# Performance work log

Hardware: AMD Instinct MI355X
Metric: run time of the kernel (lower is better)

Reference implementation:

```python
import jax, jax.numpy as jnp
import numpy as np
from jax import lax

HIDDEN = 512

def _rnn_layer(xs, W_ih, W_hh, b):
    # xs: [B,T,F] -> ys: [B,T,H]; h_t = tanh(x_t W_ih^T + b + h_{t-1} W_hh^T)
    B = xs.shape[0]
    xp = jnp.einsum('btf,hf->bth', xs, W_ih) + b  # precompute input projections
    def step(h, xp_t):
        h = jnp.tanh(xp_t + h @ W_hh.T)
        return h, h
    h0 = jnp.zeros((B, W_hh.shape[0]), dtype=xs.dtype)
    _, ys = lax.scan(step, h0, xp.transpose(1, 0, 2))  # scan over time
    return ys.transpose(1, 0, 2)


def setup_inputs() -> dict:
    key = jax.random.key(0)
    ks = jax.random.split(key, 16)
    B, T, F, H, M, C = 128, 1024, 24, HIDDEN, 1024, 8
    s = 0.05  # small init to keep tanh unsaturated
    inp = {
        'x': jax.random.normal(ks[0], (B, T, F), jnp.float32),
        'W_ih0': jax.random.normal(ks[1], (H, F), jnp.float32) * s,
        'W_hh0': jax.random.normal(ks[2], (H, H), jnp.float32) * s,
        'b_ih0': jnp.zeros((H,), jnp.float32),
        'b_hh0': jnp.zeros((H,), jnp.float32),
        'W_ih1': jax.random.normal(ks[3], (H, H), jnp.float32) * s,
        'W_hh1': jax.random.normal(ks[4], (H, H), jnp.float32) * s,
        'b_ih1': jnp.zeros((H,), jnp.float32),
        'b_hh1': jnp.zeros((H,), jnp.float32),
        'W_ih2': jax.random.normal(ks[5], (H, H), jnp.float32) * s,
        'W_hh2': jax.random.normal(ks[6], (H, H), jnp.float32) * s,
        'b_ih2': jnp.zeros((H,), jnp.float32),
        'b_hh2': jnp.zeros((H,), jnp.float32),
        'W1': jax.random.normal(ks[7], (M, H), jnp.float32) * s,
        'b1': jnp.zeros((M,), jnp.float32),
        'W2': jax.random.normal(ks[8], (C, M), jnp.float32) * s,
        'b2': jnp.zeros((C,), jnp.float32),
    }
    return inp


def reference(x, W_ih0, W_hh0, b_ih0, b_hh0, W_ih1, W_hh1, b_ih1, b_hh1,
              W_ih2, W_hh2, b_ih2, b_hh2, W1, b1, W2, b2):
    h = _rnn_layer(x, W_ih0, W_hh0, b_ih0 + b_hh0)
    h = _rnn_layer(h, W_ih1, W_hh1, b_ih1 + b_hh1)
    h = _rnn_layer(h, W_ih2, W_hh2, b_ih2 + b_hh2)
    last = h[:, -1, :]  # [B,H] last timestep of top layer
    z = last @ W1.T + b1
    z = jax.nn.silu(z)
    return z @ W2.T + b2
```

## Files before the change

kernel.cpp:

```cpp
#include <hip/hip_runtime.h>
#include <cstdint>
#include <cstddef>


typedef _Float16 half_t;
typedef __attribute__((ext_vector_type(2))) _Float16 half2_t;
typedef __attribute__((ext_vector_type(8))) _Float16 frag8;
typedef __attribute__((ext_vector_type(4))) float    frag4;

union U32H2 { unsigned u; half2_t h2; };

__device__ __forceinline__ float dot2(unsigned a, unsigned b, float c) {
#if __has_builtin(__builtin_amdgcn_fdot2)
    U32H2 ua; ua.u = a; U32H2 ub; ub.u = b;
    return __builtin_amdgcn_fdot2(ua.h2, ub.h2, c, false);
#else
    U32H2 ua; ua.u = a; U32H2 ub; ub.u = b;
    c += (float)ua.h2.x * (float)ub.h2.x;
    c += (float)ua.h2.y * (float)ub.h2.y;
    return c;
#endif
}

__device__ __forceinline__ float fast_tanh(float x) {
    float ax = __builtin_fabsf(x);
    float e  = __expf(-2.f * ax);
    float r  = (1.f - e) / (1.f + e);
    return __builtin_copysignf(r, x);
}

#define WN (512 * 512)

__global__ __launch_bounds__(256) void k_cvt(
    const float* whh0, const float* whh1, const float* whh2,
    const float* wih1, const float* wih2,
    const float* bi0, const float* bh0, const float* bi1, const float* bh1,
    const float* bi2, const float* bh2,
    half_t* w16, float* bias)
{
    int idx = blockIdx.x * 256 + threadIdx.x;
    if (idx < 5 * WN) {
        int seg = idx / WN, off = idx % WN;
        const float* s = seg == 0 ? whh0 : seg == 1 ? whh1 : seg == 2 ? whh2
                       : seg == 3 ? wih1 : wih2;
        w16[idx] = (half_t)s[off];
    } else {
        int j = idx - 5 * WN;
        if (j < 3 * 512) {
            int l = j >> 9, o = j & 511;
            const float* a = l == 0 ? bi0 : l == 1 ? bi1 : bi2;
            const float* c = l == 0 ? bh0 : l == 1 ? bh1 : bh2;
            bias[j] = a[o] + c[o];
        }
    }
}

__global__ __launch_bounds__(256) void k_xp0(
    const float* __restrict__ x, const float* __restrict__ wih0,
    const float* __restrict__ bias0, half_t* __restrict__ P)
{
    __shared__ float wl[512 * 24];
    __shared__ float xl[32 * 25];
    int tid = threadIdx.x;
    int r0  = blockIdx.x * 32;
    for (int i = tid; i < 512 * 24; i += 256) wl[i] = wih0[i];
    for (int i = tid; i < 32 * 24; i += 256) {
        int r = i / 24, f = i % 24;
        xl[r * 25 + f] = x[(size_t)(r0 + r) * 24 + f];
    }
    __syncthreads();
    int r = tid >> 3, c = tid & 7;
    float xr[24];
#pragma unroll
    for (int f = 0; f < 24; f++) xr[f] = xl[r * 25 + f];
    size_t orow = (size_t)(r0 + r) * 512;
    for (int og = 0; og < 8; og++) {
        half_t hv[8];
#pragma unroll
        for (int oj = 0; oj < 8; oj++) {
            int o = og * 64 + c * 8 + oj;
            float acc = bias0[o];
#pragma unroll
            for (int f = 0; f < 24; f++) acc = fmaf(xr[f], wl[o * 24 + f], acc);
            hv[oj] = (half_t)acc;
        }
        *(uint4*)(P + orow + og * 64 + c * 8) = *(const uint4*)hv;
    }
}

__global__ __launch_bounds__(512, 2) void k_scan(
    half_t* __restrict__ P, const half_t* __restrict__ whh)
{
    extern __shared__ char smem[];
    uint4*    wl4  = (uint4*)smem;
    unsigned* hbuf = (unsigned*)(smem + 65536);

    int o = threadIdx.x;
    int b = blockIdx.x;
    int sw = o & 7;

    const uint4* wrow = (const uint4*)(whh + (size_t)o * 512);
    uint4 wreg[56];
#pragma unroll
    for (int g = 0; g < 56; g++) wreg[g] = wrow[g];
#pragma unroll
    for (int j = 0; j < 8; j++)
        wl4[o * 8 + (j ^ sw)] = wrow[56 + j];
    if (o < 256) { hbuf[o] = 0u; hbuf[256 + o] = 0u; }
    __syncthreads();

    half_t* Pb = P + (size_t)b * 1024 * 512;
    int cur = 0;
    float xp_next = (float)Pb[o];
    for (int t = 0; t < 1024; t++) {
        float acc0 = xp_next, acc1 = 0.f, acc2 = 0.f, acc3 = 0.f;
        int tn = t + 1 < 1024 ? t + 1 : 1023;
        xp_next = (float)Pb[(size_t)tn * 512 + o];

        const uint4* h4 = (const uint4*)(hbuf + cur * 256);
#pragma unroll
        for (int g = 0; g < 56; g++) {
            uint4 hv = h4[g];
            uint4 wv = wreg[g];
            acc0 = dot2(wv.x, hv.x, acc0);
            acc1 = dot2(wv.y, hv.y, acc1);
            acc2 = dot2(wv.z, hv.z, acc2);
            acc3 = dot2(wv.w, hv.w, acc3);
        }
#pragma unroll
        for (int j = 0; j < 8; j++) {
            uint4 hv = h4[56 + j];
            uint4 wv = wl4[o * 8 + (j ^ sw)];
            acc0 = dot2(wv.x, hv.x, acc0);
            acc1 = dot2(wv.y, hv.y, acc1);
            acc2 = dot2(wv.z, hv.z, acc2);
            acc3 = dot2(wv.w, hv.w, acc3);
        }
        float hn = fast_tanh((acc0 + acc1) + (acc2 + acc3));
        half_t hh = (half_t)hn;
        ((half_t*)(hbuf + (cur ^ 1) * 256))[o] = hh;
        Pb[(size_t)t * 512 + o] = hh;
        __syncthreads();
        cur ^= 1;
    }
}

__global__ __launch_bounds__(256, 2) void k_proj(
    half_t* __restrict__ P, const half_t* __restrict__ w16,
    const float* __restrict__ bias)
{
    extern __shared__ char smem[];
    half_t* A = (half_t*)smem;
    const int AS = 520;
    int tid = threadIdx.x;
    size_t r0 = (size_t)blockIdx.x * 64;

    const uint4* Pg = (const uint4*)(P + r0 * 512);
    for (int u = tid; u < 4096; u += 256) {
        uint4 v = Pg[u];
        int row = u >> 6, col = u & 63;
        *(uint4*)(A + row * AS + col * 8) = v;
    }
    __syncthreads();

    int wave = tid >> 6, lane = tid & 63;
    int lm = lane & 15, lq = lane >> 4;

    frag4 acc[4][8];
#pragma unroll
    for (int mt = 0; mt < 4; mt++)
#pragma unroll
        for (int nt = 0; nt < 8; nt++) acc[mt][nt] = (frag4){0.f, 0.f, 0.f, 0.f};

    for (int kb = 0; kb < 16; kb++) {
        int k0 = kb * 32 + lq * 8;
        frag8 af[4];
#pragma unroll
        for (int mt = 0; mt < 4; mt++)
            af[mt] = *(const frag8*)(A + (mt * 16 + lm) * AS + k0);
        frag8 bf[8];
#pragma unroll
        for (int nt = 0; nt < 8; nt++) {
            int n = wave * 128 + nt * 16 + lm;
            bf[nt] = *(const frag8*)(w16 + (size_t)n * 512 + k0);
        }
#pragma unroll
        for (int mt = 0; mt < 4; mt++)
#pragma unroll
            for (int nt = 0; nt < 8; nt++)
                acc[mt][nt] = __builtin_amdgcn_mfma_f32_16x16x32_f16(
                    af[mt], bf[nt], acc[mt][nt], 0, 0, 0);
    }

#pragma unroll
    for (int mt = 0; mt < 4; mt++) {
        int row = mt * 16 + lq * 4;
#pragma unroll
        for (int nt = 0; nt < 8; nt++) {
            int oc = wave * 128 + nt * 16 + lm;
            float bo = bias[oc];
#pragma unroll
            for (int i = 0; i < 4; i++) {
                float v = acc[mt][nt][i] + bo;
                P[(r0 + row + i) * 512 + oc] = (half_t)v;
            }
        }
    }
}

__global__ __launch_bounds__(256) void k_head(
    const half_t* __restrict__ P, const float* __restrict__ W1,
    const float* __restrict__ b1, const float* __restrict__ W2,
    const float* __restrict__ b2, float* __restrict__ out)
{
    __shared__ float lastv[512];
    __shared__ float zl[1024];
    __shared__ float red[8][33];
    int tid = threadIdx.x, b = blockIdx.x;
    const half_t* lr = P + ((size_t)b * 1024 + 1023) * 512;
    lastv[tid]       = (float)lr[tid];
    lastv[tid + 256] = (float)lr[tid + 256];
    __syncthreads();
#pragma unroll
    for (int i = 0; i < 4; i++) {
        int m = tid + 256 * i;
        const float* wr = W1 + (size_t)m * 512;
        float acc = b1[m];
        for (int k = 0; k < 512; k += 4) {
            float4 wv = *(const float4*)(wr + k);
            acc = fmaf(wv.x, lastv[k],     acc);
            acc = fmaf(wv.y, lastv[k + 1], acc);
            acc = fmaf(wv.z, lastv[k + 2], acc);
            acc = fmaf(wv.w, lastv[k + 3], acc);
        }
        zl[m] = acc / (1.f + __expf(-acc));
    }
    __syncthreads();
    int c = tid & 7, mc = tid >> 3;
    float p = 0.f;
#pragma unroll
    for (int j = 0; j < 32; j++) {
        int m = mc * 32 + j;
        p = fmaf(zl[m], W2[c * 1024 + m], p);
    }
    red[c][mc] = p;
    __syncthreads();
    if (tid < 8) {
        float s = b2[tid];
#pragma unroll
        for (int j = 0; j < 32; j++) s += red[tid][j];
        out[b * 8 + tid] = s;
    }
}

extern "C" void kernel_launch(void* const* d_in, const int* in_sizes, int n_in,
                              void* d_out, int out_size, void* d_ws, size_t ws_size,
                              hipStream_t stream)
{
    const float* x    = (const float*)d_in[0];
    const float* wih0 = (const float*)d_in[1];
    const float* whh0 = (const float*)d_in[2];
    const float* bi0  = (const float*)d_in[3];
    const float* bh0  = (const float*)d_in[4];
    const float* wih1 = (const float*)d_in[5];
    const float* whh1 = (const float*)d_in[6];
    const float* bi1  = (const float*)d_in[7];
    const float* bh1  = (const float*)d_in[8];
    const float* wih2 = (const float*)d_in[9];
    const float* whh2 = (const float*)d_in[10];
    const float* bi2  = (const float*)d_in[11];
    const float* bh2  = (const float*)d_in[12];
    const float* W1   = (const float*)d_in[13];
    const float* b1   = (const float*)d_in[14];
    const float* W2   = (const float*)d_in[15];
    const float* b2   = (const float*)d_in[16];
    float* out = (float*)d_out;

    char* ws = (char*)d_ws;
    half_t* P    = (half_t*)ws;
    half_t* W16  = (half_t*)(ws + 134217728);
    float*  bias = (float*)(ws + 134217728 + 2621440);

    hipFuncSetAttribute((const void*)k_scan,
                        hipFuncAttributeMaxDynamicSharedMemorySize, 67584);
    hipFuncSetAttribute((const void*)k_proj,
                        hipFuncAttributeMaxDynamicSharedMemorySize, 66560);

    k_cvt<<<5126, 256, 0, stream>>>(whh0, whh1, whh2, wih1, wih2,
                                    bi0, bh0, bi1, bh1, bi2, bh2, W16, bias);
    k_xp0<<<4096, 256, 0, stream>>>(x, wih0, bias, P);
    k_scan<<<128, 512, 67584, stream>>>(P, W16 + 0 * WN);
    k_proj<<<2048, 256, 66560, stream>>>(P, W16 + 3 * WN, bias + 512);
    k_scan<<<128, 512, 67584, stream>>>(P, W16 + 1 * WN);
    k_proj<<<2048, 256, 66560, stream>>>(P, W16 + 4 * WN, bias + 1024);
    k_scan<<<128, 512, 67584, stream>>>(P, W16 + 2 * WN);
    k_head<<<128, 256, 0, stream>>>(P, W1, b1, W2, b2, out);
}
```

Measured before the change: 5.575 ms.

## Split scan recurrence K-dimension across two thread halves, keep all weights in registers

After: 10.63 ms. +90.6%, slower.

```diff
diff --git a/kernel.cpp b/kernel.cpp
--- a/kernel.cpp
+++ b/kernel.cpp
@@ -59,13 +59,16 @@
     const float* __restrict__ x, const float* __restrict__ wih0,
     const float* __restrict__ bias0, half_t* __restrict__ P)
 {
-    __shared__ float wl[512 * 24];
+    __shared__ float wl[512 * 25];
     __shared__ float xl[32 * 25];
     int tid = threadIdx.x;
     int r0  = blockIdx.x * 32;
-    for (int i = tid; i < 512 * 24; i += 256) wl[i] = wih0[i];
+    for (int i = tid; i < 512 * 24; i += 256) {
+        int o = i / 24, f = i - o * 24;
+        wl[o * 25 + f] = wih0[i];
+    }
     for (int i = tid; i < 32 * 24; i += 256) {
-        int r = i / 24, f = i % 24;
+        int r = i / 24, f = i - r * 24;
         xl[r * 25 + f] = x[(size_t)(r0 + r) * 24 + f];
     }
     __syncthreads();
@@ -81,7 +84,7 @@
             int o = og * 64 + c * 8 + oj;
             float acc = bias0[o];
 #pragma unroll
-            for (int f = 0; f < 24; f++) acc = fmaf(xr[f], wl[o * 24 + f], acc);
+            for (int f = 0; f < 24; f++) acc = fmaf(xr[f], wl[o * 25 + f], acc);
             hv[oj] = (half_t)acc;
         }
         *(uint4*)(P + orow + og * 64 + c * 8) = *(const uint4*)hv;
@@ -91,55 +94,52 @@
 __global__ __launch_bounds__(512, 2) void k_scan(
     half_t* __restrict__ P, const half_t* __restrict__ whh)
 {
-    extern __shared__ char smem[];
-    uint4*    wl4  = (uint4*)smem;
-    unsigned* hbuf = (unsigned*)(smem + 65536);
-
-    int o = threadIdx.x;
-    int b = blockIdx.x;
-    int sw = o & 7;
-
-    const uint4* wrow = (const uint4*)(whh + (size_t)o * 512);
-    uint4 wreg[56];
-#pragma unroll
-    for (int g = 0; g < 56; g++) wreg[g] = wrow[g];
-#pragma unroll
-    for (int j = 0; j < 8; j++)
-        wl4[o * 8 + (j ^ sw)] = wrow[56 + j];
-    if (o < 256) { hbuf[o] = 0u; hbuf[256 + o] = 0u; }
-    __syncthreads();
-
-    half_t* Pb = P + (size_t)b * 1024 * 512;
+    __shared__ unsigned hbuf[2][256];
+    __shared__ float2   pbuf[2][256];
+
+    int tid  = threadIdx.x;
+    int half = tid >> 8;
+    int po   = tid & 255;
+    int b    = blockIdx.x;
+
+    const uint4* w0p = (const uint4*)(whh + (size_t)(2 * po)     * 512 + half * 256);
+    const uint4* w1p = (const uint4*)(whh + (size_t)(2 * po + 1) * 512 + half * 256);
+    uint4 w0[32], w1[32];
+#pragma unroll
+    for (int g = 0; g < 32; g++) { w0[g] = w0p[g]; w1[g] = w1p[g]; }
+
+    if (half == 0) { hbuf[0][po] = 0u; hbuf[1][po] = 0u; }
+    __syncthreads();
+
+    unsigned* Pb32 = (unsigned*)(P + (size_t)b * 1024 * 512);
     int cur = 0;
-    float xp_next = (float)Pb[o];
     for (int t = 0; t < 1024; t++) {
-        float acc0 = xp_next, acc1 = 0.f, acc2 = 0.f, acc3 = 0.f;
-        int tn = t + 1 < 1024 ? t + 1 : 1023;
-        xp_next = (float)Pb[(size_t)tn * 512 + o];
-
-        const uint4* h4 = (const uint4*)(hbuf + cur * 256);
-#pragma unroll
-        for (int g = 0; g < 56; g++) {
+        unsigned xpu = Pb32[t * 256 + po];
+        const uint4* h4 = (const uint4*)hbuf[cur] + half * 32;
+        float a0 = 0.f, a1 = 0.f, a2 = 0.f, a3 = 0.f;
+        float c0 = 0.f, c1 = 0.f, c2 = 0.f, c3 = 0.f;
+#pragma unroll
+        for (int g = 0; g < 32; g++) {
             uint4 hv = h4[g];
-            uint4 wv = wreg[g];
-            acc0 = dot2(wv.x, hv.x, acc0);
-            acc1 = dot2(wv.y, hv.y, acc1);
-            acc2 = dot2(wv.z, hv.z, acc2);
-            acc3 = dot2(wv.w, hv.w, acc3);
-        }
-#pragma unroll
-        for (int j = 0; j < 8; j++) {
-            uint4 hv = h4[56 + j];
-            uint4 wv = wl4[o * 8 + (j ^ sw)];
-            acc0 = dot2(wv.x, hv.x, acc0);
-            acc1 = dot2(wv.y, hv.y, acc1);
-            acc2 = dot2(wv.z, hv.z, acc2);
-            acc3 = dot2(wv.w, hv.w, acc3);
-        }
-        float hn = fast_tanh((acc0 + acc1) + (acc2 + acc3));
-        half_t hh = (half_t)hn;
-        ((half_t*)(hbuf + (cur ^ 1) * 256))[o] = hh;
-        Pb[(size_t)t * 512 + o] = hh;
+            uint4 wv0 = w0[g], wv1 = w1[g];
+            a0 = dot2(wv0.x, hv.x, a0); a1 = dot2(wv0.y, hv.y, a1);
+            a2 = dot2(wv0.z, hv.z, a2); a3 = dot2(wv0.w, hv.w, a3);
+            c0 = dot2(wv1.x, hv.x, c0); c1 = dot2(wv1.y, hv.y, c1);
+            c2 = dot2(wv1.z, hv.z, c2); c3 = dot2(wv1.w, hv.w, c3);
+        }
+        float p0 = (a0 + a1) + (a2 + a3);
+        float p1 = (c0 + c1) + (c2 + c3);
+        pbuf[half][po] = make_float2(p0, p1);
+        __syncthreads();
+        float2 q = pbuf[half ^ 1][po];
+        U32H2 xu; xu.u = xpu;
+        float s0 = p0 + q.x + (float)xu.h2.x;
+        float s1 = p1 + q.y + (float)xu.h2.y;
+        U32H2 hu;
+        hu.h2.x = (half_t)fast_tanh(s0);
+        hu.h2.y = (half_t)fast_tanh(s1);
+        if (half == 0) hbuf[cur ^ 1][po] = hu.u;
+        else           Pb32[t * 256 + po] = hu.u;
         __syncthreads();
         cur ^= 1;
     }
@@ -281,18 +281,16 @@
     half_t* W16  = (half_t*)(ws + 134217728);
     float*  bias = (float*)(ws + 134217728 + 2621440);
 
-    hipFuncSetAttribute((const void*)k_scan,
-                        hipFuncAttributeMaxDynamicSharedMemorySize, 67584);
     hipFuncSetAttribute((const void*)k_proj,
                         hipFuncAttributeMaxDynamicSharedMemorySize, 66560);
 
     k_cvt<<<5126, 256, 0, stream>>>(whh0, whh1, whh2, wih1, wih2,
                                     bi0, bh0, bi1, bh1, bi2, bh2, W16, bias);
     k_xp0<<<4096, 256, 0, stream>>>(x, wih0, bias, P);
-    k_scan<<<128, 512, 67584, stream>>>(P, W16 + 0 * WN);
+    k_scan<<<128, 512, 0, stream>>>(P, W16 + 0 * WN);
     k_proj<<<2048, 256, 66560, stream>>>(P, W16 + 3 * WN, bias + 512);
-    k_scan<<<128, 512, 67584, stream>>>(P, W16 + 1 * WN);
+    k_scan<<<128, 512, 0, stream>>>(P, W16 + 1 * WN);
     k_proj<<<2048, 256, 66560, stream>>>(P, W16 + 4 * WN, bias + 1024);
-    k_scan<<<128, 512, 67584, stream>>>(P, W16 + 2 * WN);
+    k_scan<<<128, 512, 0, stream>>>(P, W16 + 2 * WN);
     k_head<<<128, 256, 0, stream>>>(P, W1, b1, W2, b2, out);
 }
```

## Use MFMA matrix cores for recurrent matvec in scan kernel

Applied to the files above, without the earlier changes.

Result: slower. 6.369 ms (+14.3%).

```diff
diff --git a/kernel.cpp b/kernel.cpp
--- a/kernel.cpp
+++ b/kernel.cpp
@@ -9,18 +9,6 @@
 typedef __attribute__((ext_vector_type(4))) float    frag4;
 
 union U32H2 { unsigned u; half2_t h2; };
-
-__device__ __forceinline__ float dot2(unsigned a, unsigned b, float c) {
-#if __has_builtin(__builtin_amdgcn_fdot2)
-    U32H2 ua; ua.u = a; U32H2 ub; ub.u = b;
-    return __builtin_amdgcn_fdot2(ua.h2, ub.h2, c, false);
-#else
-    U32H2 ua; ua.u = a; U32H2 ub; ub.u = b;
-    c += (float)ua.h2.x * (float)ub.h2.x;
-    c += (float)ua.h2.y * (float)ub.h2.y;
-    return c;
-#endif
-}
 
 __device__ __forceinline__ float fast_tanh(float x) {
     float ax = __builtin_fabsf(x);
@@ -59,13 +47,16 @@
     const float* __restrict__ x, const float* __restrict__ wih0,
     const float* __restrict__ bias0, half_t* __restrict__ P)
 {
-    __shared__ float wl[512 * 24];
+    __shared__ float wl[512 * 25];
     __shared__ float xl[32 * 25];
     int tid = threadIdx.x;
     int r0  = blockIdx.x * 32;
-    for (int i = tid; i < 512 * 24; i += 256) wl[i] = wih0[i];
+    for (int i = tid; i < 512 * 24; i += 256) {
+        int o = i / 24, f = i - o * 24;
+        wl[o * 25 + f] = wih0[i];
+    }
     for (int i = tid; i < 32 * 24; i += 256) {
-        int r = i / 24, f = i % 24;
+        int r = i / 24, f = i - r * 24;
         xl[r * 25 + f] = x[(size_t)(r0 + r) * 24 + f];
     }
     __syncthreads();
@@ -81,7 +72,7 @@
             int o = og * 64 + c * 8 + oj;
             float acc = bias0[o];
 #pragma unroll
-            for (int f = 0; f < 24; f++) acc = fmaf(xr[f], wl[o * 24 + f], acc);
+            for (int f = 0; f < 24; f++) acc = fmaf(xr[f], wl[o * 25 + f], acc);
             hv[oj] = (half_t)acc;
         }
         *(uint4*)(P + orow + og * 64 + c * 8) = *(const uint4*)hv;
@@ -92,54 +83,79 @@
     half_t* __restrict__ P, const half_t* __restrict__ whh)
 {
     extern __shared__ char smem[];
-    uint4*    wl4  = (uint4*)smem;
+    frag8*    wlds = (frag8*)smem;
     unsigned* hbuf = (unsigned*)(smem + 65536);
 
-    int o = threadIdx.x;
-    int b = blockIdx.x;
-    int sw = o & 7;
-
-    const uint4* wrow = (const uint4*)(whh + (size_t)o * 512);
-    uint4 wreg[56];
-#pragma unroll
-    for (int g = 0; g < 56; g++) wreg[g] = wrow[g];
-#pragma unroll
-    for (int j = 0; j < 8; j++)
-        wl4[o * 8 + (j ^ sw)] = wrow[56 + j];
-    if (o < 256) { hbuf[o] = 0u; hbuf[256 + o] = 0u; }
+    int tid  = threadIdx.x;
+    int w    = tid >> 6, lane = tid & 63;
+    int col  = lane & 15, quad = lane >> 4;
+    int b    = blockIdx.x;
+
+    frag8 areg[4][14];
+#pragma unroll
+    for (int mt = 0; mt < 4; mt++) {
+        int out = w * 64 + mt * 16 + col;
+        const half_t* wr = whh + (size_t)out * 512 + quad * 8;
+#pragma unroll
+        for (int kb = 0; kb < 14; kb++)
+            areg[mt][kb] = *(const frag8*)(wr + kb * 32);
+#pragma unroll
+        for (int i = 0; i < 2; i++)
+            wlds[(w * 8 + i * 4 + mt) * 64 + lane] = *(const frag8*)(wr + (14 + i) * 32);
+    }
+    if (tid < 256) { hbuf[tid] = 0u; hbuf[256 + tid] = 0u; }
     __syncthreads();
 
     half_t* Pb = P + (size_t)b * 1024 * 512;
+    int  out0 = w * 64 + col * 16 + quad * 4;
+    bool act  = (col < 4);
+    uint2 xq = make_uint2(0u, 0u);
+    if (act) xq = *(const uint2*)(Pb + out0);
     int cur = 0;
-    float xp_next = (float)Pb[o];
     for (int t = 0; t < 1024; t++) {
-        float acc0 = xp_next, acc1 = 0.f, acc2 = 0.f, acc3 = 0.f;
-        int tn = t + 1 < 1024 ? t + 1 : 1023;
-        xp_next = (float)Pb[(size_t)tn * 512 + o];
-
-        const uint4* h4 = (const uint4*)(hbuf + cur * 256);
-#pragma unroll
-        for (int g = 0; g < 56; g++) {
-            uint4 hv = h4[g];
-            uint4 wv = wreg[g];
-            acc0 = dot2(wv.x, hv.x, acc0);
-            acc1 = dot2(wv.y, hv.y, acc1);
-            acc2 = dot2(wv.z, hv.z, acc2);
-            acc3 = dot2(wv.w, hv.w, acc3);
-        }
-#pragma unroll
-        for (int j = 0; j < 8; j++) {
-            uint4 hv = h4[56 + j];
-            uint4 wv = wl4[o * 8 + (j ^ sw)];
-            acc0 = dot2(wv.x, hv.x, acc0);
-            acc1 = dot2(wv.y, hv.y, acc1);
-            acc2 = dot2(wv.z, hv.z, acc2);
-            acc3 = dot2(wv.w, hv.w, acc3);
-        }
-        float hn = fast_tanh((acc0 + acc1) + (acc2 + acc3));
-        half_t hh = (half_t)hn;
-        ((half_t*)(hbuf + (cur ^ 1) * 256))[o] = hh;
-        Pb[(size_t)t * 512 + o] = hh;
+        const uint4* hb4 = (const uint4*)(hbuf + cur * 256);
+        frag4 acc[4];
+#pragma unroll
+        for (int mt = 0; mt < 4; mt++) acc[mt] = (frag4){0.f, 0.f, 0.f, 0.f};
+#pragma unroll
+        for (int kb = 0; kb < 14; kb++) {
+            uint4 bu = hb4[kb * 4 + quad];
+            frag8 bf = *(const frag8*)&bu;
+#pragma unroll
+            for (int mt = 0; mt < 4; mt++)
+                acc[mt] = __builtin_amdgcn_mfma_f32_16x16x32_f16(
+                    areg[mt][kb], bf, acc[mt], 0, 0, 0);
+        }
+#pragma unroll
+        for (int i = 0; i < 2; i++) {
+            uint4 bu = hb4[(14 + i) * 4 + quad];
+            frag8 bf = *(const frag8*)&bu;
+#pragma unroll
+            for (int mt = 0; mt < 4; mt++) {
+                frag8 a = wlds[(w * 8 + i * 4 + mt) * 64 + lane];
+                acc[mt] = __builtin_amdgcn_mfma_f32_16x16x32_f16(
+                    a, bf, acc[mt], 0, 0, 0);
+            }
+        }
+        if (act) {
+            int tn = (t + 1 < 1024) ? t + 1 : 1023;
+            uint2 xn = *(const uint2*)(Pb + (size_t)tn * 512 + out0);
+            float y0 = 0.f, y1 = 0.f, y2 = 0.f, y3 = 0.f;
+#pragma unroll
+            for (int mt = 0; mt < 4; mt++)
+                if (col == mt) { y0 = acc[mt][0]; y1 = acc[mt][1];
+                                 y2 = acc[mt][2]; y3 = acc[mt][3]; }
+            U32H2 lo, hi; lo.u = xq.x; hi.u = xq.y;
+            U32H2 ho, h1;
+            ho.h2.x = (half_t)fast_tanh(y0 + (float)lo.h2.x);
+            ho.h2.y = (half_t)fast_tanh(y1 + (float)lo.h2.y);
+            h1.h2.x = (half_t)fast_tanh(y2 + (float)hi.h2.x);
+            h1.h2.y = (half_t)fast_tanh(y3 + (float)hi.h2.y);
+            uint2 hv = make_uint2(ho.u, h1.u);
+            *(uint2*)&hbuf[(cur ^ 1) * 256 + (out0 >> 1)] = hv;
+            *(uint2*)(Pb + (size_t)t * 512 + out0) = hv;
+            xq = xn;
+        }
         __syncthreads();
         cur ^= 1;
     }
@@ -158,8 +174,8 @@
     const uint4* Pg = (const uint4*)(P + r0 * 512);
     for (int u = tid; u < 4096; u += 256) {
         uint4 v = Pg[u];
-        int row = u >> 6, col = u & 63;
-        *(uint4*)(A + row * AS + col * 8) = v;
+        int row = u >> 6, c = u & 63;
+        *(uint4*)(A + row * AS + c * 8) = v;
     }
     __syncthreads();
 
```
